# Kernel tuning notes

Hardware: AMD Instinct MI355X
Metric: run time of the kernel (lower is better)

The kernel has to match this reference:

```python
import jax, jax.numpy as jnp
import numpy as np

WEIGHT = 0.85            # module init kwarg
LOW_T, HIGH_T = 0.1, 0.2  # kornia.filters.canny defaults
EPS = 1e-6


def _conv(x, k, padding):
    return jax.lax.conv_general_dilated(x, k, (1, 1), padding,
                                        dimension_numbers=('NCHW', 'OIHW', 'NCHW'))


def _gauss_kernel5():
    # kornia gaussian kernel, size 5, sigma 1
    x = jnp.arange(5, dtype=jnp.float32) - 2.0
    g = jnp.exp(-0.5 * x * x)
    g = g / g.sum()
    return jnp.outer(g, g)[None, None]  # [1,1,5,5]


_SOBEL = jnp.stack([
    jnp.array([[-1., 0., 1.], [-2., 0., 2.], [-1., 0., 1.]], jnp.float32),
    jnp.array([[-1., -2., -1.], [0., 0., 0.], [1., 2., 1.]], jnp.float32),
])[:, None]  # [2,1,3,3] unnormalized sobel (kornia spatial_gradient, normalized=False)

# 8 NMS directions in kornia's ordering: quantized angle k*45deg -> neighbor offset (dr, dc)
_OFFS = [(0, 1), (-1, 1), (-1, 0), (-1, -1), (0, -1), (1, -1), (1, 0), (1, 1)]


def _nms_kernels():
    k = np.zeros((8, 1, 3, 3), np.float32)
    for i, (dr, dc) in enumerate(_OFFS):
        k[i, 0, 1, 1] = 1.0
        k[i, 0, 1 + dr, 1 + dc] = -1.0
    return jnp.asarray(k)


_ONES3 = jnp.ones((1, 1, 3, 3), jnp.float32)


def canny_edges(img):
    """kornia.filters.canny(img)[1]; img: [N,1,H,W] -> binary edges [N,1,H,W]."""
    blurred = _conv(jnp.pad(img, ((0, 0), (0, 0), (2, 2), (2, 2)), mode='reflect'),
                    _gauss_kernel5(), 'VALID')
    grad = _conv(jnp.pad(blurred, ((0, 0), (0, 0), (1, 1), (1, 1)), mode='edge'),
                 _SOBEL, 'VALID')  # [N,2,H,W]
    gx, gy = grad[:, 0:1], grad[:, 1:2]
    mag = jnp.sqrt(gx * gx + gy * gy + EPS)
    ang = jnp.round(jnp.rad2deg(jnp.arctan2(gy, gx)) / 45.0) * 45.0
    # non-maximum suppression: (center - neighbor) along quantized direction, zero pad
    nms = _conv(mag, _nms_kernels(), [(1, 1), (1, 1)])  # [N,8,H,W]
    pos_idx = jnp.mod(ang / 45.0, 8.0).astype(jnp.int32)
    neg_idx = jnp.mod(ang / 45.0 + 4.0, 8.0).astype(jnp.int32)
    pos = jnp.take_along_axis(nms, pos_idx, axis=1)
    neg = jnp.take_along_axis(nms, neg_idx, axis=1)
    mag = mag * (jnp.minimum(pos, neg) > 0.0)
    # double threshold: weak -> 0.5, strong -> 1.0
    edges = 0.5 * (mag > LOW_T) + 0.5 * (mag > HIGH_T)

    # hysteresis: promote weak pixels 8-connected to a strong pixel, to fixed point
    def _promote(e):
        weak = (e == 0.5).astype(jnp.float32)
        strong = (e == 1.0).astype(jnp.float32)
        neigh = (_conv(strong, _ONES3, [(1, 1), (1, 1)]) > 0.0).astype(jnp.float32)
        return neigh * weak + strong, weak

    def _cond(state):
        e, e_old = state
        return jnp.any(e != e_old)

    def _body(state):
        e, _ = state
        new, weak = _promote(e)
        return new + (new == 0.0) * weak * 0.5, e

    edges, _ = jax.lax.while_loop(_cond, _body, (edges, -jnp.ones_like(edges)))
    out, _ = _promote(edges)  # final binary map: unpromoted weak pixels -> 0
    return out


def _mse(a, b):
    return jnp.mean((a - b) ** 2)


def setup_inputs() -> dict:
    key = jax.random.key(0)
    k1, k2 = jax.random.split(key)
    shape = (16, 12, 1, 256, 256)  # [B, T, C, H, W]
    pred_y = jax.random.uniform(k1, shape, dtype=jnp.float32)
    batch_y = jax.random.uniform(k2, shape, dtype=jnp.float32)
    return {"pred_y": pred_y, "batch_y": batch_y}


def reference(pred_y, batch_y):
    B, T, C, H, W = pred_y.shape
    ep = canny_edges(pred_y.reshape(B * T, C, H, W)).reshape(B, T, 1, H, W)
    et = canny_edges(batch_y.reshape(B * T, C, H, W)).reshape(B, T, 1, H, W)
    return WEIGHT * _mse(pred_y, batch_y) + (1.0 - WEIGHT) * _mse(ep, et)
```

## Files before the change

### kernel.cpp

```cpp
#include <hip/hip_runtime.h>

#define NIMG 192
#define NPIX (256*256)
#define N_TOTAL (192*65536)
typedef unsigned long long u64;

__device__ __forceinline__ int refl(int i){ i = i < 0 ? -i : i; return i > 255 ? 510 - i : i; }

__device__ __forceinline__ float dpp_shr1(float src, float oldv) {
    return __int_as_float(__builtin_amdgcn_update_dpp(
        __float_as_int(oldv), __float_as_int(src), 0x138, 0xF, 0xF, false));
}
__device__ __forceinline__ float dpp_shl1(float src, float oldv) {
    return __int_as_float(__builtin_amdgcn_update_dpp(
        __float_as_int(oldv), __float_as_int(src), 0x130, 0xF, 0xF, false));
}
__device__ __forceinline__ float dpp_shr1z(float src) {
    return __int_as_float(__builtin_amdgcn_update_dpp(
        0, __float_as_int(src), 0x138, 0xF, 0xF, true));
}
__device__ __forceinline__ float dpp_shl1z(float src) {
    return __int_as_float(__builtin_amdgcn_update_dpp(
        0, __float_as_int(src), 0x130, 0xF, 0xF, true));
}

__global__ __launch_bounds__(256, 3) void k_edges(
    const float* __restrict__ pred, const float* __restrict__ batch,
    u64* __restrict__ masks, double* __restrict__ sse)
{
    const int wv = threadIdx.x >> 6, lane = threadIdx.x & 63;
    const int band = blockIdx.x * 4 + wv;
    const int iy   = blockIdx.y;
    const int R0 = band * 32, R1 = R0 + 31;
    const bool isPred = iy < NIMG;
    const float* img  = isPred ? pred  + (size_t)iy * NPIX : batch + (size_t)(iy - NIMG) * NPIX;
    const float* oimg = isPred ? batch + (size_t)iy * NPIX : pred  + (size_t)(iy - NIMG) * NPIX;
    u64* mout = masks + (size_t)iy * 2048;
    const int mlo = isPred ? R0 : R0 + 16;
    const int mhi = isPred ? R0 + 15 : R1;

    const float W0 = 0.0544886850f, W1 = 0.2442013420f, W2 = 0.4026199469f;
    const float LO2 = 0.1f * 0.1f, HI2 = 0.2f * 0.2f;
    const float T1 = 0.41421356237f, T2 = 2.41421356237f;

    float hw0[4], hw1[4], hw2[4], hw3[4], hw4[4];
    float bo0[4], bo1[4], bo2[4];
    float mgA[4], mgB[4], mgC[4];
    float mgAL, mgAR, mgBL, mgBR, mgCL, mgCR;
    float gxp[4], gyp[4];
    float4 cur, ocur = make_float4(0.f, 0.f, 0.f, 0.f);
    float acc = 0.f;
    const float4* pi = nullptr;
    u64* mo = nullptr;

    #pragma unroll
    for (int k = 0; k < 4; ++k) {
        hw0[k]=hw1[k]=hw2[k]=hw3[k]=hw4[k]=0.f; bo0[k]=bo1[k]=bo2[k]=0.f;
        mgA[k]=mgB[k]=mgC[k]=0.f; gxp[k]=gyp[k]=0.f;
    }
    mgAL=mgAR=mgBL=mgBR=mgCL=mgCR=0.f;

    const int bstart = R0 - 6;
    cur = *(const float4*)(img + refl(bstart + 2) * 256 + (lane << 2));

    auto step = [&](const int b, const bool FAST) {
        float4 nxt;
        if (FAST) { nxt = *pi; pi += 64; }
        else      nxt = *(const float4*)(img + refl(b + 3) * 256 + (lane << 2));
        float4 onxt = ocur;
        if (b + 3 >= mlo && b + 3 <= mhi)
            onxt = *(const float4*)(oimg + ((b + 3) << 8) + (lane << 2));

        float Lz = dpp_shr1(cur.z, cur.z);
        float Lw = dpp_shr1(cur.w, cur.y);
        float Rx = dpp_shl1(cur.x, cur.z);
        float Ry = dpp_shl1(cur.y, cur.y);
        float hb[4];
        hb[0] = W0*(Lz + cur.z)  + W1*(Lw + cur.y)    + W2*cur.x;
        hb[1] = W0*(Lw + cur.w)  + W1*(cur.x + cur.z) + W2*cur.y;
        hb[2] = W0*(cur.x + Rx)  + W1*(cur.y + cur.w) + W2*cur.z;
        hb[3] = W0*(cur.y + Ry)  + W1*(cur.z + Rx)    + W2*cur.w;

        #pragma unroll
        for (int k = 0; k < 4; ++k) {
            hw0[k]=hw1[k]; hw1[k]=hw2[k]; hw2[k]=hw3[k]; hw3[k]=hw4[k]; hw4[k]=hb[k];
            float bl = W0*(hw0[k]+hw4[k]) + W1*(hw1[k]+hw3[k]) + W2*hw2[k];
            bo0[k]=bo1[k]; bo1[k]=bo2[k]; bo2[k]=bl;
        }

        const int m = b - 1;
        float t[4], u[4];
        #pragma unroll
        for (int k = 0; k < 4; ++k) {
            float lo = bo0[k], hi = bo2[k];
            if (!FAST) { if (m == 0) lo = bo1[k]; if (m == 255) hi = bo1[k]; }
            t[k] = lo + 2.f*bo1[k] + hi;
            u[k] = hi - lo;
        }
        float Lt = dpp_shr1(t[3], t[0]), Rt = dpp_shl1(t[0], t[3]);
        float Lu = dpp_shr1(u[3], u[0]), Ru = dpp_shl1(u[0], u[3]);
        float gx[4], gy[4], mg[4];
        gx[0] = t[1] - Lt;  gx[1] = t[2] - t[0];  gx[2] = t[3] - t[1];  gx[3] = Rt - t[2];
        gy[0] = Lu  + 2.f*u[0] + u[1];
        gy[1] = u[0] + 2.f*u[1] + u[2];
        gy[2] = u[1] + 2.f*u[2] + u[3];
        gy[3] = u[2] + 2.f*u[3] + Ru;
        #pragma unroll
        for (int k = 0; k < 4; ++k) mg[k] = fmaf(gx[k], gx[k], fmaf(gy[k], gy[k], 1e-6f));
        if (!FAST && (m < 0 || m > 255)) {
            #pragma unroll
            for (int k = 0; k < 4; ++k) mg[k] = 0.f;
        }
        float Lm = dpp_shr1z(mg[3]), Rm = dpp_shl1z(mg[0]);

        #pragma unroll
        for (int k = 0; k < 4; ++k) { mgA[k]=mgB[k]; mgB[k]=mgC[k]; mgC[k]=mg[k]; }
        mgAL=mgBL; mgBL=mgCL; mgCL=Lm;  mgAR=mgBR; mgBR=mgCR; mgCR=Rm;

        const int r = b - 2;
        if (FAST || (r >= R0 && r <= R1)) {
            bool wk[4], st[4];
            #pragma unroll
            for (int k = 0; k < 4; ++k) {
                float gxv = gxp[k], gyv = gyp[k];
                float ax = fabsf(gxv), ay = fabsf(gyv);
                bool horiz = (ay <= T1 * ax);
                bool vert  = (ay >= T2 * ax);
                bool d45   = ((__float_as_uint(gxv) ^ __float_as_uint(gyv)) >> 31) == 0u;
                float Bp  = (k < 3) ? mgB[k+1] : mgBR;
                float Bmv = (k > 0) ? mgB[k-1] : mgBL;
                float Ap  = (k < 3) ? mgA[k+1] : mgAR;
                float Amv = (k > 0) ? mgA[k-1] : mgAL;
                float Cp  = (k < 3) ? mgC[k+1] : mgCR;
                float Cmv = (k > 0) ? mgC[k-1] : mgCL;
                float m1 = d45 ? Ap  : Cp;   m1 = vert ? mgC[k] : m1;  m1 = horiz ? Bp  : m1;
                float m2 = d45 ? Cmv : Amv;  m2 = vert ? mgA[k] : m2;  m2 = horiz ? Bmv : m2;
                float v = mgB[k];
                bool keep = (v > m1) && (v > m2);
                wk[k] = keep && (v > LO2) && !(v > HI2);
                st[k] = keep && (v > HI2);
            }
            u64 bw0 = __ballot(wk[0]), bw1 = __ballot(wk[1]), bw2 = __ballot(wk[2]), bw3 = __ballot(wk[3]);
            u64 bs0 = __ballot(st[0]), bs1 = __ballot(st[1]), bs2 = __ballot(st[2]), bs3 = __ballot(st[3]);
            if (lane == 0) {
                u64* mrow = FAST ? mo : (mout + r * 4);
                ulonglong2 v2;
                v2.x = bw0; v2.y = bw1; ((ulonglong2*)mrow)[0] = v2;
                v2.x = bw2; v2.y = bw3; ((ulonglong2*)mrow)[1] = v2;
                v2.x = bs0; v2.y = bs1; ((ulonglong2*)(mrow + 1024))[0] = v2;
                v2.x = bs2; v2.y = bs3; ((ulonglong2*)(mrow + 1024))[1] = v2;
            }
            if (FAST) mo += 4;
        }

        if (b + 2 >= mlo && b + 2 <= mhi) {
            float dx = cur.x - ocur.x, dy = cur.y - ocur.y;
            float dz = cur.z - ocur.z, dw = cur.w - ocur.w;
            acc += dx*dx + dy*dy + dz*dz + dw*dw;
        }
        #pragma unroll
        for (int k = 0; k < 4; ++k) { gxp[k] = gx[k]; gyp[k] = gy[k]; }
        cur = nxt; ocur = onxt;
    };

    int b = bstart;
    for (; b <= R0 + 1; ++b) step(b, false);
    const int bfe = (R1 + 2 < 252) ? (R1 + 2) : 252;
    pi = (const float4*)(img + (size_t)(b + 3) * 256) + lane;
    mo = mout + (size_t)(b - 2) * 4;
    #pragma unroll 15
    for (; b <= bfe; ++b) step(b, true);
    for (; b <= R1 + 2; ++b) step(b, false);

    for (int off = 32; off; off >>= 1) acc += __shfl_down(acc, off);
    if (lane == 0)
        atomicAdd(&sse[(blockIdx.y * 2 + blockIdx.x) & 63], (double)acc);
}

__global__ __launch_bounds__(256) void k_hyst(u64* __restrict__ masks)
{
    const int im = blockIdx.x;
    u64* m = masks + (size_t)im * 2048;
    const int r = threadIdx.x;
    __shared__ u64 hd[4][256];
    __shared__ int flg[2];
    ulonglong2 wa = *(const ulonglong2*)(m + r*4);
    ulonglong2 wb = *(const ulonglong2*)(m + r*4 + 2);
    ulonglong2 sa = *(const ulonglong2*)(m + 1024 + r*4);
    ulonglong2 sb = *(const ulonglong2*)(m + 1024 + r*4 + 2);
    u64 ww0=wa.x, ww1=wa.y, ww2=wb.x, ww3=wb.y;
    u64 s0=sa.x, s1=sa.y, s2=sb.x, s3=sb.y;
    if (r < 2) flg[r] = 0;
    const int up = (r > 0) ? r - 1 : 0, dn = (r < 255) ? r + 1 : 255;
    for (int k = 0;; ++k) {
        u64 h0 = s0 | (s3 << 1) | s1;
        u64 h1 = s1 | s0 | s2;
        u64 h2 = s2 | s1 | s3;
        u64 h3 = s3 | s2 | (s0 >> 1);
        hd[0][r]=h0; hd[1][r]=h1; hd[2][r]=h2; hd[3][r]=h3;
        if (r == 0) flg[(k+1)&1] = 0;
        __syncthreads();
        u64 n0 = s0 | ((h0 | hd[0][up] | hd[0][dn]) & ww0);
        u64 n1 = s1 | ((h1 | hd[1][up] | hd[1][dn]) & ww1);
        u64 n2 = s2 | ((h2 | hd[2][up] | hd[2][dn]) & ww2);
        u64 n3 = s3 | ((h3 | hd[3][up] | hd[3][dn]) & ww3);
        bool ch = ((n0^s0) | (n1^s1) | (n2^s2) | (n3^s3)) != 0ULL;
        s0=n0; s1=n1; s2=n2; s3=n3;
        if (ch) flg[k&1] = 1;
        __syncthreads();
        if (!flg[k&1]) break;
    }
    ulonglong2 o;
    o.x = s0; o.y = s1; *(ulonglong2*)(m + 1024 + r*4)     = o;
    o.x = s2; o.y = s3; *(ulonglong2*)(m + 1024 + r*4 + 2) = o;
}

__global__ __launch_bounds__(256) void k_diff(const u64* __restrict__ masks, u64* __restrict__ cnt)
{
    const int b = blockIdx.x;
    const u64* sp = masks + (size_t)b * 2048 + 1024;
    const u64* st = masks + (size_t)(b + NIMG) * 2048 + 1024;
    int c = 0;
    for (int k = threadIdx.x; k < 1024; k += 256)
        c += __popcll(sp[k] ^ st[k]);
    for (int off = 32; off; off >>= 1) c += __shfl_down(c, off);
    __shared__ int wsum[4];
    if ((threadIdx.x & 63) == 0) wsum[threadIdx.x >> 6] = c;
    __syncthreads();
    if (threadIdx.x == 0)
        atomicAdd(cnt, (u64)(wsum[0] + wsum[1] + wsum[2] + wsum[3]));
}

__global__ void k_final(const double* __restrict__ sse, const u64* __restrict__ cnt,
                        float* __restrict__ out)
{
    double s = 0.0;
    for (int i = 0; i < 64; ++i) s += sse[i];
    float mse1 = (float)(s / (double)N_TOTAL);
    float mse2 = (float)((double)(*cnt) / (double)N_TOTAL);
    out[0] = 0.85f * mse1 + (1.0f - 0.85f) * mse2;
}

extern "C" void kernel_launch(void* const* d_in, const int* in_sizes, int n_in,
                              void* d_out, int out_size, void* d_ws, size_t ws_size,
                              hipStream_t stream)
{
    const float* pred  = (const float*)d_in[0];
    const float* batch = (const float*)d_in[1];
    float* out = (float*)d_out;
    double* sse = (double*)d_ws;
    u64* cnt    = (u64*)((char*)d_ws + 512);
    u64* masks  = (u64*)((char*)d_ws + 1024);

    hipMemsetAsync(d_ws, 0, 1024, stream);
    dim3 g1(2, 384);
    k_edges<<<g1, 256, 0, stream>>>(pred, batch, masks, sse);
    k_hyst<<<384, 256, 0, stream>>>(masks);
    k_diff<<<192, 256, 0, stream>>>(masks, cnt);
    k_final<<<1, 1, 0, stream>>>(sse, cnt, out);
}
```

Before: 76.34 us.

## Fuse hysteresis and diff kernels, streamline edge pipeline with fewer registers

The hysteresis kernel now handles a pred/target image pair per block and computes the popcount difference directly, so the separate diff kernel and its mask write and re-read go away. The edge kernel is restructured with a smaller register ring, a simplified NMS threshold test using max comparisons, and a fast path unrolled by three with pointer-based loads for the other image. The cost is that hysteresis now launches half as many blocks, each looping until the slower image of the pair converges.

```diff
diff --git a/kernel.cpp b/kernel.cpp
--- a/kernel.cpp
+++ b/kernel.cpp
@@ -37,194 +37,215 @@
     const float* oimg = isPred ? batch + (size_t)iy * NPIX : pred  + (size_t)(iy - NIMG) * NPIX;
     u64* mout = masks + (size_t)iy * 2048;
     const int mlo = isPred ? R0 : R0 + 16;
-    const int mhi = isPred ? R0 + 15 : R1;
 
     const float W0 = 0.0544886850f, W1 = 0.2442013420f, W2 = 0.4026199469f;
-    const float LO2 = 0.1f * 0.1f, HI2 = 0.2f * 0.2f;
-    const float T1 = 0.41421356237f, T2 = 2.41421356237f;
-
-    float hw0[4], hw1[4], hw2[4], hw3[4], hw4[4];
-    float bo0[4], bo1[4], bo2[4];
-    float mgA[4], mgB[4], mgC[4];
-    float mgAL, mgAR, mgBL, mgBR, mgCL, mgCR;
-    float gxp[4], gyp[4];
-    float4 cur, ocur = make_float4(0.f, 0.f, 0.f, 0.f);
+    const float LO2 = 0.01f, HI2 = 0.04f, T1 = 0.41421356237f;
+
+    float hwB[4], hwC[4], hwD[4], hwE[4], boP[4], boQ[4];
+    float mgA[4], mgB[4], mgAL, mgAR, mgBL, mgBR, gxp[4], gyp[4];
+    float4 cur;
     float acc = 0.f;
-    const float4* pi = nullptr;
+    const float4 *pi = nullptr, *po = nullptr;
     u64* mo = nullptr;
 
     #pragma unroll
     for (int k = 0; k < 4; ++k) {
-        hw0[k]=hw1[k]=hw2[k]=hw3[k]=hw4[k]=0.f; bo0[k]=bo1[k]=bo2[k]=0.f;
-        mgA[k]=mgB[k]=mgC[k]=0.f; gxp[k]=gyp[k]=0.f;
+        hwB[k]=hwC[k]=hwD[k]=hwE[k]=0.f; boP[k]=boQ[k]=0.f;
+        mgA[k]=mgB[k]=0.f; gxp[k]=gyp[k]=0.f;
     }
-    mgAL=mgAR=mgBL=mgBR=mgCL=mgCR=0.f;
-
-    const int bstart = R0 - 6;
-    cur = *(const float4*)(img + refl(bstart + 2) * 256 + (lane << 2));
-
-    auto step = [&](const int b, const bool FAST) {
-        float4 nxt;
-        if (FAST) { nxt = *pi; pi += 64; }
-        else      nxt = *(const float4*)(img + refl(b + 3) * 256 + (lane << 2));
-        float4 onxt = ocur;
-        if (b + 3 >= mlo && b + 3 <= mhi)
-            onxt = *(const float4*)(oimg + ((b + 3) << 8) + (lane << 2));
-
-        float Lz = dpp_shr1(cur.z, cur.z);
-        float Lw = dpp_shr1(cur.w, cur.y);
-        float Rx = dpp_shl1(cur.x, cur.z);
-        float Ry = dpp_shl1(cur.y, cur.y);
+    mgAL=mgAR=mgBL=mgBR=0.f;
+
+    auto donms = [&](const float mgC[4], const float CL, const float CR, u64* dst) {
+        u64 wB[4], sB[4];
+        #pragma unroll
+        for (int k = 0; k < 4; ++k) {
+            const float gxv = gxp[k], gyv = gyp[k];
+            const float ax = fabsf(gxv), ay = fabsf(gyv);
+            const bool horiz = (ay <= T1 * ax);
+            const bool vert  = (ax <= T1 * ay);
+            const bool d45 = (int)(__float_as_uint(gxv) ^ __float_as_uint(gyv)) >= 0;
+            const float Ap = (k < 3) ? mgA[k+1] : mgAR, Am = (k > 0) ? mgA[k-1] : mgAL;
+            const float Bp = (k < 3) ? mgB[k+1] : mgBR, Bm = (k > 0) ? mgB[k-1] : mgBL;
+            const float Cp = (k < 3) ? mgC[k+1] : CR,   Cm = (k > 0) ? mgC[k-1] : CL;
+            const float m1 = horiz ? Bp : (vert ? mgC[k] : (d45 ? Ap : Cp));
+            const float m2 = horiz ? Bm : (vert ? mgA[k] : (d45 ? Cm : Am));
+            const float M  = fmaxf(fmaxf(m1, m2), LO2);
+            const float v  = mgB[k];
+            wB[k] = __ballot(v > M);
+            sB[k] = __ballot(v > fmaxf(M, HI2));
+        }
+        if (lane == 0) {
+            ulonglong2 q;
+            q.x = wB[0]; q.y = wB[1]; ((ulonglong2*)dst)[0] = q;
+            q.x = wB[2]; q.y = wB[3]; ((ulonglong2*)dst)[1] = q;
+            q.x = sB[0]; q.y = sB[1]; ((ulonglong2*)(dst + 1024))[0] = q;
+            q.x = sB[2]; q.y = sB[3]; ((ulonglong2*)(dst + 1024))[1] = q;
+        }
+    };
+
+    auto steprow = [&](const int b) {
+        float4 nxt = *(const float4*)(img + (size_t)refl(b + 3) * 256 + (lane << 2));
+        const int m = b - 1, r = b - 2;
+        const bool doM = (b + 2 >= mlo) && (b + 2 <= mlo + 15);
+        float4 oc;
+        if (doM) oc = *(const float4*)(oimg + (size_t)(b + 2) * 256 + (lane << 2));
+        float Lz = dpp_shr1(cur.z, cur.z), Lw = dpp_shr1(cur.w, cur.y);
+        float Rx = dpp_shl1(cur.x, cur.z), Ry = dpp_shl1(cur.y, cur.y);
         float hb[4];
-        hb[0] = W0*(Lz + cur.z)  + W1*(Lw + cur.y)    + W2*cur.x;
-        hb[1] = W0*(Lw + cur.w)  + W1*(cur.x + cur.z) + W2*cur.y;
-        hb[2] = W0*(cur.x + Rx)  + W1*(cur.y + cur.w) + W2*cur.z;
-        hb[3] = W0*(cur.y + Ry)  + W1*(cur.z + Rx)    + W2*cur.w;
-
-        #pragma unroll
-        for (int k = 0; k < 4; ++k) {
-            hw0[k]=hw1[k]; hw1[k]=hw2[k]; hw2[k]=hw3[k]; hw3[k]=hw4[k]; hw4[k]=hb[k];
-            float bl = W0*(hw0[k]+hw4[k]) + W1*(hw1[k]+hw3[k]) + W2*hw2[k];
-            bo0[k]=bo1[k]; bo1[k]=bo2[k]; bo2[k]=bl;
-        }
-
-        const int m = b - 1;
-        float t[4], u[4];
-        #pragma unroll
-        for (int k = 0; k < 4; ++k) {
-            float lo = bo0[k], hi = bo2[k];
-            if (!FAST) { if (m == 0) lo = bo1[k]; if (m == 255) hi = bo1[k]; }
-            t[k] = lo + 2.f*bo1[k] + hi;
+        hb[0] = W0*(Lz + cur.z) + W1*(Lw + cur.y)    + W2*cur.x;
+        hb[1] = W0*(Lw + cur.w) + W1*(cur.x + cur.z) + W2*cur.y;
+        hb[2] = W0*(cur.x + Rx) + W1*(cur.y + cur.w) + W2*cur.z;
+        hb[3] = W0*(cur.y + Ry) + W1*(cur.z + Rx)    + W2*cur.w;
+        float t[4], u[4], blv[4];
+        #pragma unroll
+        for (int k = 0; k < 4; ++k) {
+            blv[k] = W0*(hwB[k] + hb[k]) + W1*(hwC[k] + hwE[k]) + W2*hwD[k];
+            float lo = (m == 0)   ? boQ[k] : boP[k];
+            float hi = (m == 255) ? boQ[k] : blv[k];
+            t[k] = lo + 2.f*boQ[k] + hi;
             u[k] = hi - lo;
         }
         float Lt = dpp_shr1(t[3], t[0]), Rt = dpp_shl1(t[0], t[3]);
         float Lu = dpp_shr1(u[3], u[0]), Ru = dpp_shl1(u[0], u[3]);
-        float gx[4], gy[4], mg[4];
-        gx[0] = t[1] - Lt;  gx[1] = t[2] - t[0];  gx[2] = t[3] - t[1];  gx[3] = Rt - t[2];
-        gy[0] = Lu  + 2.f*u[0] + u[1];
-        gy[1] = u[0] + 2.f*u[1] + u[2];
-        gy[2] = u[1] + 2.f*u[2] + u[3];
-        gy[3] = u[2] + 2.f*u[3] + Ru;
-        #pragma unroll
-        for (int k = 0; k < 4; ++k) mg[k] = fmaf(gx[k], gx[k], fmaf(gy[k], gy[k], 1e-6f));
-        if (!FAST && (m < 0 || m > 255)) {
-            #pragma unroll
-            for (int k = 0; k < 4; ++k) mg[k] = 0.f;
-        }
-        float Lm = dpp_shr1z(mg[3]), Rm = dpp_shl1z(mg[0]);
-
-        #pragma unroll
-        for (int k = 0; k < 4; ++k) { mgA[k]=mgB[k]; mgB[k]=mgC[k]; mgC[k]=mg[k]; }
-        mgAL=mgBL; mgBL=mgCL; mgCL=Lm;  mgAR=mgBR; mgBR=mgCR; mgCR=Rm;
-
-        const int r = b - 2;
-        if (FAST || (r >= R0 && r <= R1)) {
-            bool wk[4], st[4];
-            #pragma unroll
-            for (int k = 0; k < 4; ++k) {
-                float gxv = gxp[k], gyv = gyp[k];
-                float ax = fabsf(gxv), ay = fabsf(gyv);
-                bool horiz = (ay <= T1 * ax);
-                bool vert  = (ay >= T2 * ax);
-                bool d45   = ((__float_as_uint(gxv) ^ __float_as_uint(gyv)) >> 31) == 0u;
-                float Bp  = (k < 3) ? mgB[k+1] : mgBR;
-                float Bmv = (k > 0) ? mgB[k-1] : mgBL;
-                float Ap  = (k < 3) ? mgA[k+1] : mgAR;
-                float Amv = (k > 0) ? mgA[k-1] : mgAL;
-                float Cp  = (k < 3) ? mgC[k+1] : mgCR;
-                float Cmv = (k > 0) ? mgC[k-1] : mgCL;
-                float m1 = d45 ? Ap  : Cp;   m1 = vert ? mgC[k] : m1;  m1 = horiz ? Bp  : m1;
-                float m2 = d45 ? Cmv : Amv;  m2 = vert ? mgA[k] : m2;  m2 = horiz ? Bmv : m2;
-                float v = mgB[k];
-                bool keep = (v > m1) && (v > m2);
-                wk[k] = keep && (v > LO2) && !(v > HI2);
-                st[k] = keep && (v > HI2);
-            }
-            u64 bw0 = __ballot(wk[0]), bw1 = __ballot(wk[1]), bw2 = __ballot(wk[2]), bw3 = __ballot(wk[3]);
-            u64 bs0 = __ballot(st[0]), bs1 = __ballot(st[1]), bs2 = __ballot(st[2]), bs3 = __ballot(st[3]);
-            if (lane == 0) {
-                u64* mrow = FAST ? mo : (mout + r * 4);
-                ulonglong2 v2;
-                v2.x = bw0; v2.y = bw1; ((ulonglong2*)mrow)[0] = v2;
-                v2.x = bw2; v2.y = bw3; ((ulonglong2*)mrow)[1] = v2;
-                v2.x = bs0; v2.y = bs1; ((ulonglong2*)(mrow + 1024))[0] = v2;
-                v2.x = bs2; v2.y = bs3; ((ulonglong2*)(mrow + 1024))[1] = v2;
-            }
-            if (FAST) mo += 4;
-        }
-
-        if (b + 2 >= mlo && b + 2 <= mhi) {
-            float dx = cur.x - ocur.x, dy = cur.y - ocur.y;
-            float dz = cur.z - ocur.z, dw = cur.w - ocur.w;
+        float gx[4], gy[4], mgC[4];
+        gx[0] = t[1] - Lt; gx[1] = t[2] - t[0]; gx[2] = t[3] - t[1]; gx[3] = Rt - t[2];
+        gy[0] = (Lu + u[1]) + 2.f*u[0];  gy[1] = (u[0] + u[2]) + 2.f*u[1];
+        gy[2] = (u[1] + u[3]) + 2.f*u[2]; gy[3] = (u[2] + Ru) + 2.f*u[3];
+        #pragma unroll
+        for (int k = 0; k < 4; ++k) mgC[k] = fmaf(gx[k], gx[k], fmaf(gy[k], gy[k], 1e-6f));
+        if (m < 0 || m > 255) { mgC[0]=mgC[1]=mgC[2]=mgC[3]=0.f; }
+        float CL = dpp_shr1z(mgC[3]), CR = dpp_shl1z(mgC[0]);
+        if (r >= R0 && r <= R1) donms(mgC, CL, CR, mout + r * 4);
+        if (doM) {
+            float dx = cur.x - oc.x, dy = cur.y - oc.y, dz = cur.z - oc.z, dw = cur.w - oc.w;
             acc += dx*dx + dy*dy + dz*dz + dw*dw;
         }
         #pragma unroll
-        for (int k = 0; k < 4; ++k) { gxp[k] = gx[k]; gyp[k] = gy[k]; }
-        cur = nxt; ocur = onxt;
+        for (int k = 0; k < 4; ++k) {
+            hwB[k]=hwC[k]; hwC[k]=hwD[k]; hwD[k]=hwE[k]; hwE[k]=hb[k];
+            boP[k]=boQ[k]; boQ[k]=blv[k];
+            mgA[k]=mgB[k]; mgB[k]=mgC[k];
+            gxp[k]=gx[k];  gyp[k]=gy[k];
+        }
+        mgAL=mgBL; mgBL=CL; mgAR=mgBR; mgBR=CR;
+        cur = nxt;
     };
 
-    int b = bstart;
-    for (; b <= R0 + 1; ++b) step(b, false);
-    const int bfe = (R1 + 2 < 252) ? (R1 + 2) : 252;
-    pi = (const float4*)(img + (size_t)(b + 3) * 256) + lane;
-    mo = mout + (size_t)(b - 2) * 4;
-    #pragma unroll 15
-    for (; b <= bfe; ++b) step(b, true);
-    for (; b <= R1 + 2; ++b) step(b, false);
+    auto fastrow = [&](const int b) {
+        float4 nxt = *pi; pi += 64;
+        const bool doM = ((unsigned)(b + 2 - mlo) <= 15u);
+        float4 oc;
+        if (doM) oc = *po;
+        po += 64;
+        float Lz = dpp_shr1(cur.z, cur.z), Lw = dpp_shr1(cur.w, cur.y);
+        float Rx = dpp_shl1(cur.x, cur.z), Ry = dpp_shl1(cur.y, cur.y);
+        float hb[4];
+        hb[0] = W0*(Lz + cur.z) + W1*(Lw + cur.y)    + W2*cur.x;
+        hb[1] = W0*(Lw + cur.w) + W1*(cur.x + cur.z) + W2*cur.y;
+        hb[2] = W0*(cur.x + Rx) + W1*(cur.y + cur.w) + W2*cur.z;
+        hb[3] = W0*(cur.y + Ry) + W1*(cur.z + Rx)    + W2*cur.w;
+        float t[4], u[4], blv[4];
+        #pragma unroll
+        for (int k = 0; k < 4; ++k) {
+            blv[k] = W0*(hwB[k] + hb[k]) + W1*(hwC[k] + hwE[k]) + W2*hwD[k];
+            t[k] = boP[k] + 2.f*boQ[k] + blv[k];
+            u[k] = blv[k] - boP[k];
+        }
+        float Lt = dpp_shr1(t[3], t[0]), Rt = dpp_shl1(t[0], t[3]);
+        float Lu = dpp_shr1(u[3], u[0]), Ru = dpp_shl1(u[0], u[3]);
+        float gx[4], gy[4], mgC[4];
+        gx[0] = t[1] - Lt; gx[1] = t[2] - t[0]; gx[2] = t[3] - t[1]; gx[3] = Rt - t[2];
+        gy[0] = (Lu + u[1]) + 2.f*u[0];  gy[1] = (u[0] + u[2]) + 2.f*u[1];
+        gy[2] = (u[1] + u[3]) + 2.f*u[2]; gy[3] = (u[2] + Ru) + 2.f*u[3];
+        #pragma unroll
+        for (int k = 0; k < 4; ++k) mgC[k] = fmaf(gx[k], gx[k], fmaf(gy[k], gy[k], 1e-6f));
+        float CL = dpp_shr1z(mgC[3]), CR = dpp_shl1z(mgC[0]);
+        donms(mgC, CL, CR, mo); mo += 4;
+        if (doM) {
+            float dx = cur.x - oc.x, dy = cur.y - oc.y, dz = cur.z - oc.z, dw = cur.w - oc.w;
+            acc += dx*dx + dy*dy + dz*dz + dw*dw;
+        }
+        #pragma unroll
+        for (int k = 0; k < 4; ++k) {
+            hwB[k]=hwC[k]; hwC[k]=hwD[k]; hwD[k]=hwE[k]; hwE[k]=hb[k];
+            boP[k]=boQ[k]; boQ[k]=blv[k];
+            mgA[k]=mgB[k]; mgB[k]=mgC[k];
+            gxp[k]=gx[k];  gyp[k]=gy[k];
+        }
+        mgAL=mgBL; mgBL=CL; mgAR=mgBR; mgBR=CR;
+        cur = nxt;
+    };
+
+    int b = R0 - 6;
+    cur = *(const float4*)(img + (size_t)refl(b + 2) * 256 + (lane << 2));
+    for (; b <= R0 + 3; ++b) steprow(b);
+    pi = (const float4*)img  + ((R0 + 7) << 6) + lane;
+    po = (const float4*)oimg + ((R0 + 6) << 6) + lane;
+    mo = mout + (size_t)(R0 + 2) * 4;
+    const int nt = (band == 7) ? 8 : 10;
+    for (int tt = 0; tt < nt; ++tt) {
+        fastrow(b); fastrow(b + 1); fastrow(b + 2); b += 3;
+    }
+    for (; b <= R1 + 2; ++b) steprow(b);
 
     for (int off = 32; off; off >>= 1) acc += __shfl_down(acc, off);
     if (lane == 0)
         atomicAdd(&sse[(blockIdx.y * 2 + blockIdx.x) & 63], (double)acc);
 }
 
-__global__ __launch_bounds__(256) void k_hyst(u64* __restrict__ masks)
-{
-    const int im = blockIdx.x;
-    u64* m = masks + (size_t)im * 2048;
+__global__ __launch_bounds__(256) void k_hyst(const u64* __restrict__ masks,
+                                              u64* __restrict__ cnt)
+{
+    const int pr = blockIdx.x;
+    const u64* mp = masks + (size_t)pr * 2048;
+    const u64* mt = masks + (size_t)(pr + NIMG) * 2048;
     const int r = threadIdx.x;
-    __shared__ u64 hd[4][256];
+    __shared__ u64 hd[8][256];
     __shared__ int flg[2];
-    ulonglong2 wa = *(const ulonglong2*)(m + r*4);
-    ulonglong2 wb = *(const ulonglong2*)(m + r*4 + 2);
-    ulonglong2 sa = *(const ulonglong2*)(m + 1024 + r*4);
-    ulonglong2 sb = *(const ulonglong2*)(m + 1024 + r*4 + 2);
-    u64 ww0=wa.x, ww1=wa.y, ww2=wb.x, ww3=wb.y;
-    u64 s0=sa.x, s1=sa.y, s2=sb.x, s3=sb.y;
+    __shared__ int wsum[4];
+    ulonglong2 a0 = ((const ulonglong2*)(mp + r*4))[0];
+    ulonglong2 a1 = ((const ulonglong2*)(mp + r*4))[1];
+    ulonglong2 a2 = ((const ulonglong2*)(mp + 1024 + r*4))[0];
+    ulonglong2 a3 = ((const ulonglong2*)(mp + 1024 + r*4))[1];
+    ulonglong2 b0 = ((const ulonglong2*)(mt + r*4))[0];
+    ulonglong2 b1 = ((const ulonglong2*)(mt + r*4))[1];
+    ulonglong2 b2 = ((const ulonglong2*)(mt + 1024 + r*4))[0];
+    ulonglong2 b3 = ((const ulonglong2*)(mt + 1024 + r*4))[1];
+    u64 pw0=a0.x, pw1=a0.y, pw2=a1.x, pw3=a1.y;
+    u64 ps0=a2.x, ps1=a2.y, ps2=a3.x, ps3=a3.y;
+    u64 tw0=b0.x, tw1=b0.y, tw2=b1.x, tw3=b1.y;
+    u64 ts0=b2.x, ts1=b2.y, ts2=b3.x, ts3=b3.y;
     if (r < 2) flg[r] = 0;
-    const int up = (r > 0) ? r - 1 : 0, dn = (r < 255) ? r + 1 : 255;
+    const int up = r ? r - 1 : 0, dn = (r < 255) ? r + 1 : 255;
     for (int k = 0;; ++k) {
-        u64 h0 = s0 | (s3 << 1) | s1;
-        u64 h1 = s1 | s0 | s2;
-        u64 h2 = s2 | s1 | s3;
-        u64 h3 = s3 | s2 | (s0 >> 1);
-        hd[0][r]=h0; hd[1][r]=h1; hd[2][r]=h2; hd[3][r]=h3;
-        if (r == 0) flg[(k+1)&1] = 0;
+        u64 hp0 = ps0 | (ps3 << 1) | ps1;
+        u64 hp1 = ps1 | ps0 | ps2;
+        u64 hp2 = ps2 | ps1 | ps3;
+        u64 hp3 = ps3 | ps2 | (ps0 >> 1);
+        u64 ht0 = ts0 | (ts3 << 1) | ts1;
+        u64 ht1 = ts1 | ts0 | ts2;
+        u64 ht2 = ts2 | ts1 | ts3;
+        u64 ht3 = ts3 | ts2 | (ts0 >> 1);
+        hd[0][r]=hp0; hd[1][r]=hp1; hd[2][r]=hp2; hd[3][r]=hp3;
+        hd[4][r]=ht0; hd[5][r]=ht1; hd[6][r]=ht2; hd[7][r]=ht3;
+        if (r == 0) flg[(k + 1) & 1] = 0;
         __syncthreads();
-        u64 n0 = s0 | ((h0 | hd[0][up] | hd[0][dn]) & ww0);
-        u64 n1 = s1 | ((h1 | hd[1][up] | hd[1][dn]) & ww1);
-        u64 n2 = s2 | ((h2 | hd[2][up] | hd[2][dn]) & ww2);
-        u64 n3 = s3 | ((h3 | hd[3][up] | hd[3][dn]) & ww3);
-        bool ch = ((n0^s0) | (n1^s1) | (n2^s2) | (n3^s3)) != 0ULL;
-        s0=n0; s1=n1; s2=n2; s3=n3;
-        if (ch) flg[k&1] = 1;
+        u64 n0 = ps0 | ((hp0 | hd[0][up] | hd[0][dn]) & pw0);
+        u64 n1 = ps1 | ((hp1 | hd[1][up] | hd[1][dn]) & pw1);
+        u64 n2 = ps2 | ((hp2 | hd[2][up] | hd[2][dn]) & pw2);
+        u64 n3 = ps3 | ((hp3 | hd[3][up] | hd[3][dn]) & pw3);
+        u64 m0 = ts0 | ((ht0 | hd[4][up] | hd[4][dn]) & tw0);
+        u64 m1 = ts1 | ((ht1 | hd[5][up] | hd[5][dn]) & tw1);
+        u64 m2 = ts2 | ((ht2 | hd[6][up] | hd[6][dn]) & tw2);
+        u64 m3 = ts3 | ((ht3 | hd[7][up] | hd[7][dn]) & tw3);
+        u64 chg = (n0^ps0)|(n1^ps1)|(n2^ps2)|(n3^ps3)|(m0^ts0)|(m1^ts1)|(m2^ts2)|(m3^ts3);
+        ps0=n0; ps1=n1; ps2=n2; ps3=n3; ts0=m0; ts1=m1; ts2=m2; ts3=m3;
+        if (chg) flg[k & 1] = 1;
         __syncthreads();
-        if (!flg[k&1]) break;
+        if (!flg[k & 1]) break;
     }
-    ulonglong2 o;
-    o.x = s0; o.y = s1; *(ulonglong2*)(m + 1024 + r*4)     = o;
-    o.x = s2; o.y = s3; *(ulonglong2*)(m + 1024 + r*4 + 2) = o;
-}
-
-__global__ __launch_bounds__(256) void k_diff(const u64* __restrict__ masks, u64* __restrict__ cnt)
-{
-    const int b = blockIdx.x;
-    const u64* sp = masks + (size_t)b * 2048 + 1024;
-    const u64* st = masks + (size_t)(b + NIMG) * 2048 + 1024;
-    int c = 0;
-    for (int k = threadIdx.x; k < 1024; k += 256)
-        c += __popcll(sp[k] ^ st[k]);
+    int c = __popcll(ps0^ts0) + __popcll(ps1^ts1) + __popcll(ps2^ts2) + __popcll(ps3^ts3);
     for (int off = 32; off; off >>= 1) c += __shfl_down(c, off);
-    __shared__ int wsum[4];
     if ((threadIdx.x & 63) == 0) wsum[threadIdx.x >> 6] = c;
     __syncthreads();
     if (threadIdx.x == 0)
@@ -255,7 +276,6 @@
     hipMemsetAsync(d_ws, 0, 1024, stream);
     dim3 g1(2, 384);
     k_edges<<<g1, 256, 0, stream>>>(pred, batch, masks, sse);
-    k_hyst<<<384, 256, 0, stream>>>(masks);
-    k_diff<<<192, 256, 0, stream>>>(masks, cnt);
+    k_hyst<<<192, 256, 0, stream>>>(masks, cnt);
     k_final<<<1, 1, 0, stream>>>(sse, cnt, out);
 }
```

After: 69.48 us. -9.0%, faster.
